# Optimization experiments

Hardware: AMD Instinct MI355X
Metric: run time of the kernel (lower is better)

Reference implementation:

```python
import jax, jax.numpy as jnp
import numpy as np

B, C, H, W = 2, 512, 48, 48
HEADS = 8
REDUCTION = 4
DPH = max(C // REDUCTION // HEADS, 1)   # 16
TOTAL = DPH * HEADS                      # 128
EPS_NORM = 1e-12
EPS_BN = 1e-5


def setup_inputs() -> dict:
    key = jax.random.key(0)
    ks = jax.random.split(key, 6)
    x = jax.random.normal(ks[0], (B, C, H, W), dtype=jnp.float32)
    # 1x1 convs stored as [out_ch, in_ch] matrices
    w_qkv = jax.random.normal(ks[1], (3 * TOTAL, C), dtype=jnp.float32) * (1.0 / np.sqrt(C))
    w_out = jax.random.normal(ks[2], (C, TOTAL), dtype=jnp.float32) * (1.0 / np.sqrt(TOTAL))
    temperature = jnp.ones((HEADS, 1, 1), dtype=jnp.float32)
    bn_gamma = jnp.ones((C,), dtype=jnp.float32)
    bn_beta = jnp.zeros((C,), dtype=jnp.float32)
    return {"x": x, "w_qkv": w_qkv, "temperature": temperature,
            "w_out": w_out, "bn_gamma": bn_gamma, "bn_beta": bn_beta}


def _l2norm(t):
    # F.normalize(t, dim=-1): t / max(||t||_2, eps)
    n = jnp.sqrt(jnp.sum(t * t, axis=-1, keepdims=True))
    return t / jnp.maximum(n, EPS_NORM)


def reference(x, w_qkv, temperature, w_out, bn_gamma, bn_beta):
    b, c, h, w = x.shape
    n = h * w
    # qkv 1x1 conv: [b, 3*TOTAL, h, w]
    qkv = jnp.einsum('bchw,oc->bohw', x, w_qkv)
    q, k, v = jnp.split(qkv, 3, axis=1)
    # [b, heads, dph, n] -> [b, heads, n, dph]
    def heads_tokens(t):
        return t.reshape(b, HEADS, DPH, n).transpose(0, 1, 3, 2)
    q = _l2norm(heads_tokens(q))
    k = _l2norm(heads_tokens(k))
    v = heads_tokens(v)
    # [b, heads, n, n]
    attn = jnp.einsum('bhnd,bhmd->bhnm', q, k) * temperature[None]
    attn = jax.nn.softmax(attn, axis=-1)
    out = jnp.einsum('bhnm,bhmd->bhnd', attn, v)          # [b, heads, n, dph]
    out = out.transpose(0, 1, 3, 2).reshape(b, TOTAL, h, w)
    # project_out: 1x1 conv then BatchNorm2d (training-mode batch stats)
    out = jnp.einsum('bthw,ct->bchw', out, w_out)
    mean = jnp.mean(out, axis=(0, 2, 3))
    var = jnp.mean((out - mean[None, :, None, None]) ** 2, axis=(0, 2, 3))
    out = (out - mean[None, :, None, None]) * jax.lax.rsqrt(var + EPS_BN)[None, :, None, None]
    out = out * bn_gamma[None, :, None, None] + bn_beta[None, :, None, None]
    return out
```

## Files before the change

### kernel.cpp

```cpp
#include <hip/hip_runtime.h>

#define NB 2
#define CC 512
#define NN 2304
#define NH 8
#define DD 16
#define TT 128
#define O3 384

typedef __attribute__((ext_vector_type(4))) float f32x4;
typedef __attribute__((ext_vector_type(8))) __bf16 bf16x8;
typedef __attribute__((ext_vector_type(4))) __bf16 bf16x4;
typedef __attribute__((ext_vector_type(4))) _Float16 f16x4;

#define OFF_Q  0u
#define OFF_K  1179648u
#define OFF_VT 2359296u
#define OFF_AO 3538944u

__global__ __launch_bounds__(256) void k1_qkv(
    const float* __restrict__ x, const float* __restrict__ wqkv,
    _Float16* __restrict__ Q, _Float16* __restrict__ K, _Float16* __restrict__ VT)
{
    int ob = blockIdx.x, nt = blockIdx.y, b = blockIdx.z;
    int lane = threadIdx.x & 63, wave = threadIdx.x >> 6;
    int quad = lane >> 4, col = lane & 15;
    int n0 = nt * 64 + wave * 16;
    int o0 = ob * 32;

    f32x4 acc0 = {0.f, 0.f, 0.f, 0.f};
    f32x4 acc1 = {0.f, 0.f, 0.f, 0.f};

    const float* ax  = x + (size_t)b * CC * NN + (size_t)(quad * 8) * NN + n0 + col;
    const float* w0p = wqkv + (size_t)(o0 + col) * CC + quad * 8;
    const float* w1p = w0p + 16 * CC;

    float ca[8];
#pragma unroll
    for (int j = 0; j < 8; j++) ca[j] = ax[(size_t)j * NN];
    f32x4 cw0a = *(const f32x4*)(w0p);
    f32x4 cw0b = *(const f32x4*)(w0p + 4);
    f32x4 cw1a = *(const f32x4*)(w1p);
    f32x4 cw1b = *(const f32x4*)(w1p + 4);

#pragma unroll
    for (int ks = 0; ks < 16; ks++) {
        float na[8];
        f32x4 nw0a, nw0b, nw1a, nw1b;
        if (ks < 15) {
            const float* axn = ax + (size_t)(ks + 1) * 32 * NN;
#pragma unroll
            for (int j = 0; j < 8; j++) na[j] = axn[(size_t)j * NN];
            nw0a = *(const f32x4*)(w0p + (ks + 1) * 32);
            nw0b = *(const f32x4*)(w0p + (ks + 1) * 32 + 4);
            nw1a = *(const f32x4*)(w1p + (ks + 1) * 32);
            nw1b = *(const f32x4*)(w1p + (ks + 1) * 32 + 4);
        }
        bf16x8 af, wf0, wf1;
#pragma unroll
        for (int j = 0; j < 8; j++) af[j] = (__bf16)ca[j];
#pragma unroll
        for (int j = 0; j < 4; j++) {
            wf0[j]     = (__bf16)cw0a[j];
            wf0[j + 4] = (__bf16)cw0b[j];
            wf1[j]     = (__bf16)cw1a[j];
            wf1[j + 4] = (__bf16)cw1b[j];
        }
        acc0 = __builtin_amdgcn_mfma_f32_16x16x32_bf16(af, wf0, acc0, 0, 0, 0);
        acc1 = __builtin_amdgcn_mfma_f32_16x16x32_bf16(af, wf1, acc1, 0, 0, 0);
#pragma unroll
        for (int j = 0; j < 8; j++) ca[j] = na[j];
        cw0a = nw0a; cw0b = nw0b; cw1a = nw1a; cw1b = nw1b;
    }

#pragma unroll
    for (int s = 0; s < 2; s++) {
        int oc = o0 + s * 16 + col;
        int d = oc & 15, h = (oc >> 4) & 7, kind = oc >> 7;
        f32x4 v = (s == 0) ? acc0 : acc1;
        if (kind < 2) {
            float ss0 = v[0] * v[0], ss1 = v[1] * v[1], ss2 = v[2] * v[2], ss3 = v[3] * v[3];
#pragma unroll
            for (int m = 1; m < 16; m <<= 1) {
                ss0 += __shfl_xor(ss0, m);
                ss1 += __shfl_xor(ss1, m);
                ss2 += __shfl_xor(ss2, m);
                ss3 += __shfl_xor(ss3, m);
            }
            v[0] *= 1.0f / fmaxf(sqrtf(ss0), 1e-12f);
            v[1] *= 1.0f / fmaxf(sqrtf(ss1), 1e-12f);
            v[2] *= 1.0f / fmaxf(sqrtf(ss2), 1e-12f);
            v[3] *= 1.0f / fmaxf(sqrtf(ss3), 1e-12f);
            _Float16* dst = (kind == 0 ? Q : K) + (size_t)(b * NH + h) * NN * DD;
#pragma unroll
            for (int r = 0; r < 4; r++) {
                int n = n0 + quad * 4 + r;
                dst[(size_t)n * DD + d] = (_Float16)v[r];
            }
        } else {
            f16x4 pk;
#pragma unroll
            for (int r = 0; r < 4; r++) pk[r] = (_Float16)v[r];
            int n = n0 + quad * 4;
            *(f16x4*)(VT + (size_t)((b * NH + h) * DD + d) * NN + n) = pk;
        }
    }
}

__global__ __launch_bounds__(512) void k2_attn(
    const _Float16* __restrict__ Q, const _Float16* __restrict__ K,
    const _Float16* __restrict__ VT, const float* __restrict__ temp,
    __bf16* __restrict__ AO)
{
    __shared__ float Osh[8][16][64];
    __shared__ float Lsh[8][64];

    int qt = blockIdx.x, bh = blockIdx.y;
    int lane = threadIdx.x & 63, wave = threadIdx.x >> 6;
    int quad = lane >> 4, col = lane & 15;
    int kbase = wave * 288;
    int qbase = qt * 64;

    const _Float16* Qb = Q + (size_t)bh * NN * DD;
    float tl2 = temp[bh & 7] * 1.4426950408889634f;

    f16x4 qf0 = *(const f16x4*)(Qb + (size_t)(qbase +  0 + col) * DD + quad * 4);
    f16x4 qf1 = *(const f16x4*)(Qb + (size_t)(qbase + 16 + col) * DD + quad * 4);
    f16x4 qf2 = *(const f16x4*)(Qb + (size_t)(qbase + 32 + col) * DD + quad * 4);
    f16x4 qf3 = *(const f16x4*)(Qb + (size_t)(qbase + 48 + col) * DD + quad * 4);

    f32x4 oa0 = {0.f,0.f,0.f,0.f}, oa1 = {0.f,0.f,0.f,0.f};
    f32x4 oa2 = {0.f,0.f,0.f,0.f}, oa3 = {0.f,0.f,0.f,0.f};
    float la0 = 0.f, la1 = 0.f, la2 = 0.f, la3 = 0.f;
    const f32x4 zc = {0.f,0.f,0.f,0.f};

    const _Float16* kp = K + (size_t)bh * NN * DD + (size_t)(kbase + col) * DD + quad * 4;
    const _Float16* vp = VT + (size_t)bh * DD * NN + (size_t)col * NN + kbase + quad * 4;

    f16x4 kfa = *(const f16x4*)(kp);
    f16x4 kfb = *(const f16x4*)(kp + 16 * DD);
    f16x4 vfa = *(const f16x4*)(vp);
    f16x4 vfb = *(const f16x4*)(vp + 16);

#define K2_CHUNK(KF, VF)                                                        \
    {                                                                           \
        f32x4 s0 = __builtin_amdgcn_mfma_f32_16x16x16f16(KF, qf0, zc, 0, 0, 0); \
        f32x4 s1 = __builtin_amdgcn_mfma_f32_16x16x16f16(KF, qf1, zc, 0, 0, 0); \
        f32x4 s2 = __builtin_amdgcn_mfma_f32_16x16x16f16(KF, qf2, zc, 0, 0, 0); \
        f32x4 s3 = __builtin_amdgcn_mfma_f32_16x16x16f16(KF, qf3, zc, 0, 0, 0); \
        f16x4 p0, p1, p2, p3;                                                   \
        _Pragma("unroll")                                                       \
        for (int r = 0; r < 4; ++r) {                                           \
            float e0 = __builtin_amdgcn_exp2f(tl2 * s0[r]);                     \
            float e1 = __builtin_amdgcn_exp2f(tl2 * s1[r]);                     \
            float e2 = __builtin_amdgcn_exp2f(tl2 * s2[r]);                     \
            float e3 = __builtin_amdgcn_exp2f(tl2 * s3[r]);                     \
            p0[r] = (_Float16)e0; la0 += e0;                                    \
            p1[r] = (_Float16)e1; la1 += e1;                                    \
            p2[r] = (_Float16)e2; la2 += e2;                                    \
            p3[r] = (_Float16)e3; la3 += e3;                                    \
        }                                                                       \
        oa0 = __builtin_amdgcn_mfma_f32_16x16x16f16(VF, p0, oa0, 0, 0, 0);      \
        oa1 = __builtin_amdgcn_mfma_f32_16x16x16f16(VF, p1, oa1, 0, 0, 0);      \
        oa2 = __builtin_amdgcn_mfma_f32_16x16x16f16(VF, p2, oa2, 0, 0, 0);      \
        oa3 = __builtin_amdgcn_mfma_f32_16x16x16f16(VF, p3, oa3, 0, 0, 0);      \
    }

    for (int g = 0; g < 9; ++g) {
        f16x4 kna, knb, vna, vnb;
        if (g < 8) {
            kna = *(const f16x4*)(kp + 32 * DD);
            knb = *(const f16x4*)(kp + 48 * DD);
            vna = *(const f16x4*)(vp + 32);
            vnb = *(const f16x4*)(vp + 48);
        }
        K2_CHUNK(kfa, vfa)
        K2_CHUNK(kfb, vfb)
        kfa = kna; kfb = knb; vfa = vna; vfb = vnb;
        kp += 32 * DD; vp += 32;
    }
#undef K2_CHUNK

    la0 += __shfl_xor(la0, 16); la0 += __shfl_xor(la0, 32);
    la1 += __shfl_xor(la1, 16); la1 += __shfl_xor(la1, 32);
    la2 += __shfl_xor(la2, 16); la2 += __shfl_xor(la2, 32);
    la3 += __shfl_xor(la3, 16); la3 += __shfl_xor(la3, 32);

#pragma unroll
    for (int r = 0; r < 4; ++r) {
        Osh[wave][quad * 4 + r][ 0 + col] = oa0[r];
        Osh[wave][quad * 4 + r][16 + col] = oa1[r];
        Osh[wave][quad * 4 + r][32 + col] = oa2[r];
        Osh[wave][quad * 4 + r][48 + col] = oa3[r];
    }
    float lv = (quad == 0) ? la0 : (quad == 1) ? la1 : (quad == 2) ? la2 : la3;
    Lsh[wave][quad * 16 + col] = lv;
    __syncthreads();

    int t = threadIdx.x;
    int q = t & 63, dg = t >> 6;
    float l = 0.f;
#pragma unroll
    for (int w = 0; w < 8; ++w) l += Lsh[w][q];
    float inv = 1.0f / l;
    float o0 = 0.f, o1 = 0.f;
#pragma unroll
    for (int w = 0; w < 8; ++w) {
        o0 += Osh[w][dg * 2 + 0][q];
        o1 += Osh[w][dg * 2 + 1][q];
    }
    int b = bh >> 3, h = bh & 7;
    __bf16* dst = AO + (size_t)(b * NN + qbase + q) * TT + h * DD + dg * 2;
    dst[0] = (__bf16)(o0 * inv);
    dst[1] = (__bf16)(o1 * inv);
}

__global__ __launch_bounds__(256) void k3_proj(
    const __bf16* __restrict__ AO, const float* __restrict__ wout,
    float* __restrict__ out)
{
    int cb = blockIdx.x, nt = blockIdx.y, b = blockIdx.z;
    int lane = threadIdx.x & 63, wave = threadIdx.x >> 6;
    int quad = lane >> 4, col = lane & 15;
    int n0 = nt * 64 + wave * 16, c0 = cb * 32;

    f32x4 acc0 = {0.f, 0.f, 0.f, 0.f};
    f32x4 acc1 = {0.f, 0.f, 0.f, 0.f};

    const __bf16* ab  = AO + (size_t)(b * NN + n0 + col) * TT + quad * 8;
    const float*  wb0 = wout + (size_t)(c0 + col) * TT + quad * 8;
    const float*  wb1 = wb0 + 16 * TT;
#pragma unroll
    for (int ks = 0; ks < 4; ks++) {
        bf16x8 a = *(const bf16x8*)(ab + ks * 32);
        f32x4 wA = *(const f32x4*)(wb0 + ks * 32);
        f32x4 wB = *(const f32x4*)(wb0 + ks * 32 + 4);
        f32x4 wC = *(const f32x4*)(wb1 + ks * 32);
        f32x4 wD = *(const f32x4*)(wb1 + ks * 32 + 4);
        bf16x8 w0, w1;
#pragma unroll
        for (int j = 0; j < 4; j++) {
            w0[j]     = (__bf16)wA[j];
            w0[j + 4] = (__bf16)wB[j];
            w1[j]     = (__bf16)wC[j];
            w1[j + 4] = (__bf16)wD[j];
        }
        acc0 = __builtin_amdgcn_mfma_f32_16x16x32_bf16(a, w0, acc0, 0, 0, 0);
        acc1 = __builtin_amdgcn_mfma_f32_16x16x32_bf16(a, w1, acc1, 0, 0, 0);
    }
#pragma unroll
    for (int s = 0; s < 2; s++) {
        int c = c0 + s * 16 + col;
        float* dst = out + (size_t)(b * CC + c) * NN + n0 + quad * 4;
        *(f32x4*)dst = (s == 0) ? acc0 : acc1;
    }
}

__global__ __launch_bounds__(256) void k4_bn(
    float* __restrict__ out, const float* __restrict__ gamma,
    const float* __restrict__ beta)
{
    int c = blockIdx.x;
    int t = threadIdx.x;
    float vals[18];
    float s = 0.f, q = 0.f;
#pragma unroll
    for (int i = 0; i < 18; i++) {
        int j = i * 256 + t;
        int b = j / NN, n = j % NN;
        float v = out[(size_t)(b * CC + c) * NN + n];
        vals[i] = v; s += v; q += v * v;
    }
#pragma unroll
    for (int m = 1; m < 64; m <<= 1) { s += __shfl_xor(s, m); q += __shfl_xor(q, m); }
    __shared__ float rs[4], rq[4];
    int lane = t & 63, wave = t >> 6;
    if (lane == 0) { rs[wave] = s; rq[wave] = q; }
    __syncthreads();
    s = rs[0] + rs[1] + rs[2] + rs[3];
    q = rq[0] + rq[1] + rq[2] + rq[3];
    float mean = s * (1.0f / 4608.0f);
    float var = q * (1.0f / 4608.0f) - mean * mean;
    float sc = rsqrtf(var + 1e-5f) * gamma[c];
    float sh = beta[c] - mean * sc;
#pragma unroll
    for (int i = 0; i < 18; i++) {
        int j = i * 256 + t;
        int b = j / NN, n = j % NN;
        out[(size_t)(b * CC + c) * NN + n] = vals[i] * sc + sh;
    }
}

extern "C" void kernel_launch(void* const* d_in, const int* in_sizes, int n_in,
                              void* d_out, int out_size, void* d_ws, size_t ws_size,
                              hipStream_t stream) {
    const float* x     = (const float*)d_in[0];
    const float* wqkv  = (const float*)d_in[1];
    const float* temp  = (const float*)d_in[2];
    const float* wout  = (const float*)d_in[3];
    const float* gamma = (const float*)d_in[4];
    const float* beta  = (const float*)d_in[5];
    float* out = (float*)d_out;
    char* ws = (char*)d_ws;

    _Float16* Q  = (_Float16*)(ws + OFF_Q);
    _Float16* K  = (_Float16*)(ws + OFF_K);
    _Float16* VT = (_Float16*)(ws + OFF_VT);
    __bf16*   AO = (__bf16*)(ws + OFF_AO);

    k1_qkv<<<dim3(12, 36, 2), 256, 0, stream>>>(x, wqkv, Q, K, VT);
    k2_attn<<<dim3(36, 16), 512, 0, stream>>>(Q, K, VT, temp, AO);
    k3_proj<<<dim3(16, 36, 2), 256, 0, stream>>>(AO, wout, out);
    k4_bn<<<512, 256, 0, stream>>>(out, gamma, beta);
}
```

Measured before the change: 143.8 us.

## Stage x tile in LDS for QKV GEMM and offload softmax row sums to MFMA

The QKV projection kernel now loads a 64-token by 512-channel slab of x into shared memory as bf16 once per block, and each block computes 64 output channels instead of 32, which halves the grid and reduces repeated strided global reads of x. In the attention kernel, the temperature scale is folded into Q once up front. Exponentials are packed to fp16 with cvt_pkrtz, and the softmax denominators are accumulated with an extra MFMA against a ones matrix instead of scalar adds and shuffles. This trades VALU work for more MFMA issue and a large LDS allocation (about 66 KB) that may limit occupancy. It also adds rounding from the fp16 temperature scaling and the truncating conversions.

After: 148.5 us. 3.2% more time.

```diff
diff --git a/kernel.cpp b/kernel.cpp
--- a/kernel.cpp
+++ b/kernel.cpp
@@ -12,6 +12,12 @@
 typedef __attribute__((ext_vector_type(8))) __bf16 bf16x8;
 typedef __attribute__((ext_vector_type(4))) __bf16 bf16x4;
 typedef __attribute__((ext_vector_type(4))) _Float16 f16x4;
+typedef __attribute__((ext_vector_type(2))) __fp16 hf16x2;
+
+union hf2pair {
+    hf16x2 h[2];
+    f16x4  v;
+};
 
 #define OFF_Q  0u
 #define OFF_K  1179648u
@@ -22,62 +28,78 @@
     const float* __restrict__ x, const float* __restrict__ wqkv,
     _Float16* __restrict__ Q, _Float16* __restrict__ K, _Float16* __restrict__ VT)
 {
+    __shared__ __bf16 As[64][520];
     int ob = blockIdx.x, nt = blockIdx.y, b = blockIdx.z;
-    int lane = threadIdx.x & 63, wave = threadIdx.x >> 6;
+    int tid = threadIdx.x;
+    int lane = tid & 63, wave = tid >> 6;
     int quad = lane >> 4, col = lane & 15;
-    int n0 = nt * 64 + wave * 16;
-    int o0 = ob * 32;
-
-    f32x4 acc0 = {0.f, 0.f, 0.f, 0.f};
-    f32x4 acc1 = {0.f, 0.f, 0.f, 0.f};
-
-    const float* ax  = x + (size_t)b * CC * NN + (size_t)(quad * 8) * NN + n0 + col;
+    int n0 = nt * 64;
+    int o0 = ob * 64;
+
+    {
+        int cb = tid >> 4;
+        int nq = (tid & 15) * 4;
+#pragma unroll
+        for (int it = 0; it < 32; ++it) {
+            int c = it * 16 + cb;
+            f32x4 v = *(const f32x4*)(x + ((size_t)b * CC + c) * NN + n0 + nq);
+            As[nq + 0][c] = (__bf16)v[0];
+            As[nq + 1][c] = (__bf16)v[1];
+            As[nq + 2][c] = (__bf16)v[2];
+            As[nq + 3][c] = (__bf16)v[3];
+        }
+    }
+    __syncthreads();
+
+    f32x4 acc0 = {0.f,0.f,0.f,0.f}, acc1 = {0.f,0.f,0.f,0.f};
+    f32x4 acc2 = {0.f,0.f,0.f,0.f}, acc3 = {0.f,0.f,0.f,0.f};
+
+    int nrow = wave * 16 + col;
     const float* w0p = wqkv + (size_t)(o0 + col) * CC + quad * 8;
     const float* w1p = w0p + 16 * CC;
-
-    float ca[8];
-#pragma unroll
-    for (int j = 0; j < 8; j++) ca[j] = ax[(size_t)j * NN];
-    f32x4 cw0a = *(const f32x4*)(w0p);
-    f32x4 cw0b = *(const f32x4*)(w0p + 4);
-    f32x4 cw1a = *(const f32x4*)(w1p);
-    f32x4 cw1b = *(const f32x4*)(w1p + 4);
+    const float* w2p = w0p + 32 * CC;
+    const float* w3p = w0p + 48 * CC;
+
+    f32x4 cw0a = *(const f32x4*)(w0p),     cw0b = *(const f32x4*)(w0p + 4);
+    f32x4 cw1a = *(const f32x4*)(w1p),     cw1b = *(const f32x4*)(w1p + 4);
+    f32x4 cw2a = *(const f32x4*)(w2p),     cw2b = *(const f32x4*)(w2p + 4);
+    f32x4 cw3a = *(const f32x4*)(w3p),     cw3b = *(const f32x4*)(w3p + 4);
 
 #pragma unroll
     for (int ks = 0; ks < 16; ks++) {
-        float na[8];
-        f32x4 nw0a, nw0b, nw1a, nw1b;
+        f32x4 nw0a, nw0b, nw1a, nw1b, nw2a, nw2b, nw3a, nw3b;
         if (ks < 15) {
-            const float* axn = ax + (size_t)(ks + 1) * 32 * NN;
-#pragma unroll
-            for (int j = 0; j < 8; j++) na[j] = axn[(size_t)j * NN];
             nw0a = *(const f32x4*)(w0p + (ks + 1) * 32);
             nw0b = *(const f32x4*)(w0p + (ks + 1) * 32 + 4);
             nw1a = *(const f32x4*)(w1p + (ks + 1) * 32);
             nw1b = *(const f32x4*)(w1p + (ks + 1) * 32 + 4);
-        }
-        bf16x8 af, wf0, wf1;
-#pragma unroll
-        for (int j = 0; j < 8; j++) af[j] = (__bf16)ca[j];
+            nw2a = *(const f32x4*)(w2p + (ks + 1) * 32);
+            nw2b = *(const f32x4*)(w2p + (ks + 1) * 32 + 4);
+            nw3a = *(const f32x4*)(w3p + (ks + 1) * 32);
+            nw3b = *(const f32x4*)(w3p + (ks + 1) * 32 + 4);
+        }
+        bf16x8 a = *(const bf16x8*)(&As[nrow][quad * 8 + ks * 32]);
+        bf16x8 wf0, wf1, wf2, wf3;
 #pragma unroll
         for (int j = 0; j < 4; j++) {
-            wf0[j]     = (__bf16)cw0a[j];
-            wf0[j + 4] = (__bf16)cw0b[j];
-            wf1[j]     = (__bf16)cw1a[j];
-            wf1[j + 4] = (__bf16)cw1b[j];
-        }
-        acc0 = __builtin_amdgcn_mfma_f32_16x16x32_bf16(af, wf0, acc0, 0, 0, 0);
-        acc1 = __builtin_amdgcn_mfma_f32_16x16x32_bf16(af, wf1, acc1, 0, 0, 0);
-#pragma unroll
-        for (int j = 0; j < 8; j++) ca[j] = na[j];
+            wf0[j] = (__bf16)cw0a[j]; wf0[j + 4] = (__bf16)cw0b[j];
+            wf1[j] = (__bf16)cw1a[j]; wf1[j + 4] = (__bf16)cw1b[j];
+            wf2[j] = (__bf16)cw2a[j]; wf2[j + 4] = (__bf16)cw2b[j];
+            wf3[j] = (__bf16)cw3a[j]; wf3[j + 4] = (__bf16)cw3b[j];
+        }
+        acc0 = __builtin_amdgcn_mfma_f32_16x16x32_bf16(a, wf0, acc0, 0, 0, 0);
+        acc1 = __builtin_amdgcn_mfma_f32_16x16x32_bf16(a, wf1, acc1, 0, 0, 0);
+        acc2 = __builtin_amdgcn_mfma_f32_16x16x32_bf16(a, wf2, acc2, 0, 0, 0);
+        acc3 = __builtin_amdgcn_mfma_f32_16x16x32_bf16(a, wf3, acc3, 0, 0, 0);
         cw0a = nw0a; cw0b = nw0b; cw1a = nw1a; cw1b = nw1b;
-    }
-
-#pragma unroll
-    for (int s = 0; s < 2; s++) {
+        cw2a = nw2a; cw2b = nw2b; cw3a = nw3a; cw3b = nw3b;
+    }
+
+#pragma unroll
+    for (int s = 0; s < 4; s++) {
         int oc = o0 + s * 16 + col;
         int d = oc & 15, h = (oc >> 4) & 7, kind = oc >> 7;
-        f32x4 v = (s == 0) ? acc0 : acc1;
+        f32x4 v = (s == 0) ? acc0 : (s == 1) ? acc1 : (s == 2) ? acc2 : acc3;
         if (kind < 2) {
             float ss0 = v[0] * v[0], ss1 = v[1] * v[1], ss2 = v[2] * v[2], ss3 = v[3] * v[3];
 #pragma unroll
@@ -94,14 +116,14 @@
             _Float16* dst = (kind == 0 ? Q : K) + (size_t)(b * NH + h) * NN * DD;
 #pragma unroll
             for (int r = 0; r < 4; r++) {
-                int n = n0 + quad * 4 + r;
+                int n = n0 + wave * 16 + quad * 4 + r;
                 dst[(size_t)n * DD + d] = (_Float16)v[r];
             }
         } else {
             f16x4 pk;
 #pragma unroll
             for (int r = 0; r < 4; r++) pk[r] = (_Float16)v[r];
-            int n = n0 + quad * 4;
+            int n = n0 + wave * 16 + quad * 4;
             *(f16x4*)(VT + (size_t)((b * NH + h) * DD + d) * NN + n) = pk;
         }
     }
@@ -123,15 +145,22 @@
 
     const _Float16* Qb = Q + (size_t)bh * NN * DD;
     float tl2 = temp[bh & 7] * 1.4426950408889634f;
+    _Float16 tl2h = (_Float16)tl2;
 
     f16x4 qf0 = *(const f16x4*)(Qb + (size_t)(qbase +  0 + col) * DD + quad * 4);
     f16x4 qf1 = *(const f16x4*)(Qb + (size_t)(qbase + 16 + col) * DD + quad * 4);
     f16x4 qf2 = *(const f16x4*)(Qb + (size_t)(qbase + 32 + col) * DD + quad * 4);
     f16x4 qf3 = *(const f16x4*)(Qb + (size_t)(qbase + 48 + col) * DD + quad * 4);
+#pragma unroll
+    for (int j = 0; j < 4; j++) {
+        qf0[j] *= tl2h; qf1[j] *= tl2h; qf2[j] *= tl2h; qf3[j] *= tl2h;
+    }
+    const f16x4 onesf = {(_Float16)1.f, (_Float16)1.f, (_Float16)1.f, (_Float16)1.f};
 
     f32x4 oa0 = {0.f,0.f,0.f,0.f}, oa1 = {0.f,0.f,0.f,0.f};
     f32x4 oa2 = {0.f,0.f,0.f,0.f}, oa3 = {0.f,0.f,0.f,0.f};
-    float la0 = 0.f, la1 = 0.f, la2 = 0.f, la3 = 0.f;
+    f32x4 lc0 = {0.f,0.f,0.f,0.f}, lc1 = {0.f,0.f,0.f,0.f};
+    f32x4 lc2 = {0.f,0.f,0.f,0.f}, lc3 = {0.f,0.f,0.f,0.f};
     const f32x4 zc = {0.f,0.f,0.f,0.f};
 
     const _Float16* kp = K + (size_t)bh * NN * DD + (size_t)(kbase + col) * DD + quad * 4;
@@ -148,18 +177,28 @@
         f32x4 s1 = __builtin_amdgcn_mfma_f32_16x16x16f16(KF, qf1, zc, 0, 0, 0); \
         f32x4 s2 = __builtin_amdgcn_mfma_f32_16x16x16f16(KF, qf2, zc, 0, 0, 0); \
         f32x4 s3 = __builtin_amdgcn_mfma_f32_16x16x16f16(KF, qf3, zc, 0, 0, 0); \
-        f16x4 p0, p1, p2, p3;                                                   \
-        _Pragma("unroll")                                                       \
-        for (int r = 0; r < 4; ++r) {                                           \
-            float e0 = __builtin_amdgcn_exp2f(tl2 * s0[r]);                     \
-            float e1 = __builtin_amdgcn_exp2f(tl2 * s1[r]);                     \
-            float e2 = __builtin_amdgcn_exp2f(tl2 * s2[r]);                     \
-            float e3 = __builtin_amdgcn_exp2f(tl2 * s3[r]);                     \
-            p0[r] = (_Float16)e0; la0 += e0;                                    \
-            p1[r] = (_Float16)e1; la1 += e1;                                    \
-            p2[r] = (_Float16)e2; la2 += e2;                                    \
-            p3[r] = (_Float16)e3; la3 += e3;                                    \
-        }                                                                       \
+        hf2pair u0, u1, u2, u3;                                                 \
+        u0.h[0] = __builtin_amdgcn_cvt_pkrtz(__builtin_amdgcn_exp2f(s0[0]),     \
+                                             __builtin_amdgcn_exp2f(s0[1]));    \
+        u0.h[1] = __builtin_amdgcn_cvt_pkrtz(__builtin_amdgcn_exp2f(s0[2]),     \
+                                             __builtin_amdgcn_exp2f(s0[3]));    \
+        u1.h[0] = __builtin_amdgcn_cvt_pkrtz(__builtin_amdgcn_exp2f(s1[0]),     \
+                                             __builtin_amdgcn_exp2f(s1[1]));    \
+        u1.h[1] = __builtin_amdgcn_cvt_pkrtz(__builtin_amdgcn_exp2f(s1[2]),     \
+                                             __builtin_amdgcn_exp2f(s1[3]));    \
+        u2.h[0] = __builtin_amdgcn_cvt_pkrtz(__builtin_amdgcn_exp2f(s2[0]),     \
+                                             __builtin_amdgcn_exp2f(s2[1]));    \
+        u2.h[1] = __builtin_amdgcn_cvt_pkrtz(__builtin_amdgcn_exp2f(s2[2]),     \
+                                             __builtin_amdgcn_exp2f(s2[3]));    \
+        u3.h[0] = __builtin_amdgcn_cvt_pkrtz(__builtin_amdgcn_exp2f(s3[0]),     \
+                                             __builtin_amdgcn_exp2f(s3[1]));    \
+        u3.h[1] = __builtin_amdgcn_cvt_pkrtz(__builtin_amdgcn_exp2f(s3[2]),     \
+                                             __builtin_amdgcn_exp2f(s3[3]));    \
+        f16x4 p0 = u0.v, p1 = u1.v, p2 = u2.v, p3 = u3.v;                       \
+        lc0 = __builtin_amdgcn_mfma_f32_16x16x16f16(onesf, p0, lc0, 0, 0, 0);   \
+        lc1 = __builtin_amdgcn_mfma_f32_16x16x16f16(onesf, p1, lc1, 0, 0, 0);   \
+        lc2 = __builtin_amdgcn_mfma_f32_16x16x16f16(onesf, p2, lc2, 0, 0, 0);   \
+        lc3 = __builtin_amdgcn_mfma_f32_16x16x16f16(onesf, p3, lc3, 0, 0, 0);   \
         oa0 = __builtin_amdgcn_mfma_f32_16x16x16f16(VF, p0, oa0, 0, 0, 0);      \
         oa1 = __builtin_amdgcn_mfma_f32_16x16x16f16(VF, p1, oa1, 0, 0, 0);      \
         oa2 = __builtin_amdgcn_mfma_f32_16x16x16f16(VF, p2, oa2, 0, 0, 0);      \
@@ -181,11 +220,6 @@
     }
 #undef K2_CHUNK
 
-    la0 += __shfl_xor(la0, 16); la0 += __shfl_xor(la0, 32);
-    la1 += __shfl_xor(la1, 16); la1 += __shfl_xor(la1, 32);
-    la2 += __shfl_xor(la2, 16); la2 += __shfl_xor(la2, 32);
-    la3 += __shfl_xor(la3, 16); la3 += __shfl_xor(la3, 32);
-
 #pragma unroll
     for (int r = 0; r < 4; ++r) {
         Osh[wave][quad * 4 + r][ 0 + col] = oa0[r];
@@ -193,7 +227,7 @@
         Osh[wave][quad * 4 + r][32 + col] = oa2[r];
         Osh[wave][quad * 4 + r][48 + col] = oa3[r];
     }
-    float lv = (quad == 0) ? la0 : (quad == 1) ? la1 : (quad == 2) ? la2 : la3;
+    float lv = (quad == 0) ? lc0[0] : (quad == 1) ? lc1[0] : (quad == 2) ? lc2[0] : lc3[0];
     Lsh[wave][quad * 16 + col] = lv;
     __syncthreads();
 
@@ -308,7 +342,7 @@
     _Float16* VT = (_Float16*)(ws + OFF_VT);
     __bf16*   AO = (__bf16*)(ws + OFF_AO);
 
-    k1_qkv<<<dim3(12, 36, 2), 256, 0, stream>>>(x, wqkv, Q, K, VT);
+    k1_qkv<<<dim3(6, 36, 2), 256, 0, stream>>>(x, wqkv, Q, K, VT);
     k2_attn<<<dim3(36, 16), 512, 0, stream>>>(Q, K, VT, temp, AO);
     k3_proj<<<dim3(16, 36, 2), 256, 0, stream>>>(AO, wout, out);
     k4_bn<<<512, 256, 0, stream>>>(out, gamma, beta);
```
